# Kernel tuning notes

Measured on AMD Instinct MI355X. Metric: run time of the kernel, lower is better.

## Reference

```python
import jax, jax.numpy as jnp
import numpy as np

SOBEL_X = jnp.array([[-1., 0., 1.], [-2., 0., 2.], [-1., 0., 1.]], dtype=jnp.float32).reshape(1, 1, 3, 3)
SOBEL_Y = jnp.array([[-1., -2., -1.], [0., 0., 0.], [1., 2., 1.]], dtype=jnp.float32).reshape(1, 1, 3, 3)
KERNEL_MASK = jnp.ones((1, 1, 3, 3), dtype=jnp.float32)


def _conv(x, k):
    # x: (N,1,H,W), k: (1,1,3,3), SAME padding (matches torch padding=1)
    return jax.lax.conv_general_dilated(
        x, k, window_strides=(1, 1), padding='SAME',
        dimension_numbers=('NCHW', 'OIHW', 'NCHW'))


def setup_inputs() -> dict:
    key = jax.random.key(0)
    k1, k2, k3 = jax.random.split(key, 3)
    shape = (2, 6, 512, 512, 8)  # (B, T, H, W, F)
    prediction = jax.random.normal(k1, shape, dtype=jnp.float32)
    target = jax.random.normal(k2, shape, dtype=jnp.float32)
    mask = jax.random.randint(k3, shape, 0, 2, dtype=jnp.int32)
    return {"prediction": prediction, "target": target, "mask": mask}


def reference(prediction, target, mask):
    B, T, H, W, F = prediction.shape
    # (B,T,H,W,F) -> (B*T*F, 1, H, W)
    def to_nchw(x):
        return x.transpose(0, 1, 4, 2, 3).reshape(B * T * F, 1, H, W)

    mask_r = to_nchw(mask.astype(jnp.float32))
    pred_r = to_nchw(prediction)
    tgt_r = to_nchw(target)

    valid = (_conv(mask_r, KERNEL_MASK) == 9.0).astype(prediction.dtype)

    gx_p = _conv(pred_r, SOBEL_X) * valid
    gy_p = _conv(pred_r, SOBEL_Y) * valid
    gx_t = _conv(tgt_r, SOBEL_X) * valid
    gy_t = _conv(tgt_r, SOBEL_Y) * valid

    # mode == 'l1'
    loss = jnp.abs(gx_p - gx_t) + jnp.abs(gy_p - gy_t)
    # (B*T*F,1,H,W) -> (B,T,H,W,F)
    return loss.reshape(B, T, F, H, W).transpose(0, 1, 3, 4, 2)
```

## Files before the change

kernel.cpp:

```cpp
#include <hip/hip_runtime.h>


constexpr int H = 512, W = 512, F = 8;
constexpr int IMAGES = 12;
constexpr int SPAN  = 128;
constexpr int NSPAN = W / SPAN;
constexpr int ORWS  = 6;
constexpr int SRWS  = 8;
constexpr int STRIPS = (H + ORWS - 1) / ORWS;
constexpr int NB = IMAGES * NSPAN * STRIPS;
constexpr int UROW = 2 * SPAN + 4;

typedef float f32x4 __attribute__((ext_vector_type(4)));

__global__ __launch_bounds__(512) void sobel_loss_kernel(
    const float* __restrict__ pred,
    const float* __restrict__ tgt,
    const int*   __restrict__ mask,
    float*       __restrict__ out)
{
    __shared__ float4         dls[SRWS * UROW];
    __shared__ unsigned short mls[SRWS * UROW];

    const int tid  = threadIdx.x;
    const int l    = tid & 63;
    const int wv   = tid >> 6;

    const int b0  = blockIdx.x;
    const int bid = (b0 & 7) * (NB >> 3) + (b0 >> 3);

    const int img   = bid / (NSPAN * STRIPS);
    const int rest  = bid - img * (NSPAN * STRIPS);
    const int span  = rest / STRIPS;
    const int strip = rest - span * STRIPS;

    const int r0 = strip * ORWS;
    const int w0 = span * SPAN;

    const size_t ibase = (size_t)img * ((size_t)H * W * F);

    {
        const int gr  = r0 - 1 + wv;
        const int grc = gr < 0 ? 0 : (gr >= H ? H - 1 : gr);
        const bool rv = (gr >= 0) & (gr < H);
        const size_t rowf = ibase + (size_t)grc * (W * F) + (size_t)w0 * F;

        float4 P[4], T[4]; int4 M[4];
#pragma unroll
        for (int k = 0; k < 4; ++k) {
            const size_t o = rowf + (size_t)k * 256 + l * 4;
            P[k] = *(const float4*)(pred + o);
            T[k] = *(const float4*)(tgt  + o);
            M[k] = *(const int4*)(mask + o);
        }

        float4 EP = make_float4(0.f,0.f,0.f,0.f), ET = EP;
        int4   EM = make_int4(0,0,0,0);
        const bool left = (l < 2);
        const int  qe   = l & 1;
        const int  pxg  = left ? (w0 - 1) : (w0 + SPAN);
        const bool ib   = (pxg >= 0) & (pxg < W);
        if (l < 4) {
            const int pxc = ib ? pxg : 0;
            const size_t o = ibase + (size_t)grc * (W * F) + (size_t)pxc * F + qe * 4;
            EP = *(const float4*)(pred + o);
            ET = *(const float4*)(tgt  + o);
            EM = *(const int4*)(mask + o);
        }

        float4* drow = dls + wv * UROW;
        unsigned short* mrow = mls + wv * UROW;
#pragma unroll
        for (int k = 0; k < 4; ++k) {
            const int u = 2 + k * 64 + l;
            drow[u] = make_float4(P[k].x - T[k].x, P[k].y - T[k].y,
                                  P[k].z - T[k].z, P[k].w - T[k].w);
            const unsigned bits = (unsigned)(M[k].x | (M[k].y << 1) |
                                             (M[k].z << 2) | (M[k].w << 3));
            mrow[u] = (unsigned short)(rv ? bits : 0u);
        }
        if (l < 4) {
            const int u = left ? qe : (2 + 2 * SPAN + qe);
            drow[u] = make_float4(EP.x - ET.x, EP.y - ET.y,
                                  EP.z - ET.z, EP.w - ET.w);
            const unsigned bits = (unsigned)(EM.x | (EM.y << 1) |
                                             (EM.z << 2) | (EM.w << 3));
            mrow[u] = (unsigned short)((rv && ib) ? bits : 0u);
        }
    }

    __syncthreads();

#pragma unroll
    for (int pass = 0; pass < 3; ++pass) {
        const int ot = tid + pass * 512;
        const int ol = ot >> 8;
        const int uo = ot & 255;
        const int ro = r0 + ol;
        if (ro < H) {
            const int bc = (ol + 1) * UROW + 2 + uo;

            const float4 a0 = dls[bc - UROW - 2];
            const float4 a1 = dls[bc - UROW];
            const float4 a2 = dls[bc - UROW + 2];
            const unsigned mA = (unsigned)mls[bc - UROW - 2] &
                                (unsigned)mls[bc - UROW] &
                                (unsigned)mls[bc - UROW + 2];
            const float4 b0r = dls[bc - 2];
            const float4 b1r = dls[bc];
            const float4 b2r = dls[bc + 2];
            const unsigned mB = (unsigned)mls[bc - 2] &
                                (unsigned)mls[bc] &
                                (unsigned)mls[bc + 2];
            const float4 c0 = dls[bc + UROW - 2];
            const float4 c1 = dls[bc + UROW];
            const float4 c2 = dls[bc + UROW + 2];
            const unsigned mC = (unsigned)mls[bc + UROW - 2] &
                                (unsigned)mls[bc + UROW] &
                                (unsigned)mls[bc + UROW + 2];

            const unsigned vm = mA & mB & mC;

            f32x4 o;
#define COMP(cc, bit)                                                          \
            {                                                                  \
                const float hx0 = a2.cc - a0.cc;                               \
                const float hx1 = b2r.cc - b0r.cc;                             \
                const float hx2 = c2.cc - c0.cc;                               \
                const float hs0 = a0.cc + 2.f * a1.cc + a2.cc;                 \
                const float hs2 = c0.cc + 2.f * c1.cc + c2.cc;                 \
                const float gx = hx0 + 2.f * hx1 + hx2;                        \
                const float gy = hs2 - hs0;                                    \
                o.cc = (vm & (1u << bit)) ? (fabsf(gx) + fabsf(gy)) : 0.f;     \
            }
            COMP(x, 0) COMP(y, 1) COMP(z, 2) COMP(w, 3)
#undef COMP

            float* const op = out + ibase + ((size_t)ro * W + w0) * F + uo * 4;
            __builtin_nontemporal_store(o, (f32x4*)op);
        }
    }
}

extern "C" void kernel_launch(void* const* d_in, const int* in_sizes, int n_in,
                              void* d_out, int out_size, void* d_ws, size_t ws_size,
                              hipStream_t stream) {
    const float* pred = (const float*)d_in[0];
    const float* tgt  = (const float*)d_in[1];
    const int*   mask = (const int*)d_in[2];
    float*       out  = (float*)d_out;

    sobel_loss_kernel<<<NB, 512, 0, stream>>>(pred, tgt, mask, out);
}
```

Before: 314.2 us.

## Stream rows through shared-memory ring buffer with register prefetch per block

Replaces the one-shot strip kernel, which reloads two halo rows for every six output rows, with blocks that walk 64-row vertical chunks of a 64-pixel span. Input rows go into a 10-slot shared ring, and the next rows are prefetched into registers while the current rows are computed. This cuts redundant halo reads from about 33% to about 3% and overlaps global loads with compute. In exchange it adds two barriers per iteration, launches fewer and smaller blocks (768 blocks of 256 threads), and uses ordinary stores in place of nontemporal ones.

```diff
diff --git a/kernel.cpp b/kernel.cpp
--- a/kernel.cpp
+++ b/kernel.cpp
@@ -3,129 +3,154 @@
 
 constexpr int H = 512, W = 512, F = 8;
 constexpr int IMAGES = 12;
-constexpr int SPAN  = 128;
+constexpr int SPAN  = 64;
 constexpr int NSPAN = W / SPAN;
-constexpr int ORWS  = 6;
-constexpr int SRWS  = 8;
-constexpr int STRIPS = (H + ORWS - 1) / ORWS;
-constexpr int NB = IMAGES * NSPAN * STRIPS;
-constexpr int UROW = 2 * SPAN + 4;
+constexpr int VCH   = 64;
+constexpr int NVCH  = H / VCH;
+constexpr int NB    = IMAGES * NSPAN * NVCH;
+constexpr int RING  = 10;
+constexpr int STEP  = 8;
+constexpr int ITERS = VCH / STEP;
+constexpr int UROW  = 2 * SPAN + 4;
 
 typedef float f32x4 __attribute__((ext_vector_type(4)));
 
-__global__ __launch_bounds__(512) void sobel_loss_kernel(
+struct RowReg {
+    float4 p0, p1, t0, t1, hp, ht;
+    int4   m0, m1, hm;
+};
+
+__device__ __forceinline__ int pack4(const int4 m) {
+    return m.x | (m.y << 1) | (m.z << 2) | (m.w << 3);
+}
+
+__device__ __forceinline__ float4 sub4(const float4 a, const float4 b) {
+    return make_float4(a.x - b.x, a.y - b.y, a.z - b.z, a.w - b.w);
+}
+
+__device__ __forceinline__ void row_load(
+    RowReg& R, const float* __restrict__ pred, const float* __restrict__ tgt,
+    const int* __restrict__ mask, size_t ibase, int gr, int w0, int l)
+{
+    const int grc = gr < 0 ? 0 : (gr > H - 1 ? H - 1 : gr);
+    const size_t rb = ibase + (size_t)grc * (W * F) + (size_t)w0 * F;
+    const int lo = l * 4;
+    R.p0 = *(const float4*)(pred + rb + lo);
+    R.p1 = *(const float4*)(pred + rb + lo + 256);
+    R.t0 = *(const float4*)(tgt  + rb + lo);
+    R.t1 = *(const float4*)(tgt  + rb + lo + 256);
+    R.m0 = *(const int4*)(mask + rb + lo);
+    R.m1 = *(const int4*)(mask + rb + lo + 256);
+    R.hp = make_float4(0.f, 0.f, 0.f, 0.f);
+    R.ht = R.hp;
+    R.hm = make_int4(0, 0, 0, 0);
+    if (l < 4) {
+        const int side = l >> 1, hq = l & 1;
+        const int px  = side ? w0 + SPAN : w0 - 1;
+        const int pxc = px < 0 ? 0 : (px > W - 1 ? W - 1 : px);
+        const size_t hb = ibase + (size_t)grc * (W * F) + (size_t)pxc * F + hq * 4;
+        R.hp = *(const float4*)(pred + hb);
+        R.ht = *(const float4*)(tgt  + hb);
+        R.hm = *(const int4*)(mask + hb);
+    }
+}
+
+__device__ __forceinline__ void row_write(
+    const RowReg& R, float4* __restrict__ dls, unsigned* __restrict__ mls,
+    int slot, int gr, int w0, int l)
+{
+    const bool rv = (gr >= 0) & (gr < H);
+    float4*   drow = dls + slot * UROW;
+    unsigned* mrow = mls + slot * UROW;
+    drow[2 + l]  = sub4(R.p0, R.t0);
+    drow[66 + l] = sub4(R.p1, R.t1);
+    mrow[2 + l]  = rv ? (unsigned)pack4(R.m0) : 0u;
+    mrow[66 + l] = rv ? (unsigned)pack4(R.m1) : 0u;
+    if (l < 4) {
+        const int side = l >> 1, hq = l & 1;
+        const int px = side ? w0 + SPAN : w0 - 1;
+        const bool ib = (px >= 0) & (px < W);
+        const int u = side ? (2 + 2 * SPAN + hq) : hq;
+        drow[u] = sub4(R.hp, R.ht);
+        mrow[u] = (rv && ib) ? (unsigned)pack4(R.hm) : 0u;
+    }
+}
+
+__global__ __launch_bounds__(256, 3) void sobel_loss_kernel(
     const float* __restrict__ pred,
     const float* __restrict__ tgt,
     const int*   __restrict__ mask,
     float*       __restrict__ out)
 {
-    __shared__ float4         dls[SRWS * UROW];
-    __shared__ unsigned short mls[SRWS * UROW];
+    __shared__ float4   dls[RING * UROW];
+    __shared__ unsigned mls[RING * UROW];
 
-    const int tid  = threadIdx.x;
-    const int l    = tid & 63;
-    const int wv   = tid >> 6;
+    const int tid = threadIdx.x;
+    const int l   = tid & 63;
+    const int wv  = tid >> 6;
 
-    const int b0  = blockIdx.x;
-    const int bid = (b0 & 7) * (NB >> 3) + (b0 >> 3);
-
-    const int img   = bid / (NSPAN * STRIPS);
-    const int rest  = bid - img * (NSPAN * STRIPS);
-    const int span  = rest / STRIPS;
-    const int strip = rest - span * STRIPS;
-
-    const int r0 = strip * ORWS;
-    const int w0 = span * SPAN;
+    const int bid  = blockIdx.x;
+    const int img  = bid >> 6;
+    const int rest = bid & 63;
+    const int span = rest >> 3;
+    const int vch  = rest & 7;
+    const int w0   = span * SPAN;
+    const int v0   = vch * VCH;
 
     const size_t ibase = (size_t)img * ((size_t)H * W * F);
 
-    {
-        const int gr  = r0 - 1 + wv;
-        const int grc = gr < 0 ? 0 : (gr >= H ? H - 1 : gr);
-        const bool rv = (gr >= 0) & (gr < H);
-        const size_t rowf = ibase + (size_t)grc * (W * F) + (size_t)w0 * F;
-
-        float4 P[4], T[4]; int4 M[4];
-#pragma unroll
-        for (int k = 0; k < 4; ++k) {
-            const size_t o = rowf + (size_t)k * 256 + l * 4;
-            P[k] = *(const float4*)(pred + o);
-            T[k] = *(const float4*)(tgt  + o);
-            M[k] = *(const int4*)(mask + o);
-        }
-
-        float4 EP = make_float4(0.f,0.f,0.f,0.f), ET = EP;
-        int4   EM = make_int4(0,0,0,0);
-        const bool left = (l < 2);
-        const int  qe   = l & 1;
-        const int  pxg  = left ? (w0 - 1) : (w0 + SPAN);
-        const bool ib   = (pxg >= 0) & (pxg < W);
-        if (l < 4) {
-            const int pxc = ib ? pxg : 0;
-            const size_t o = ibase + (size_t)grc * (W * F) + (size_t)pxc * F + qe * 4;
-            EP = *(const float4*)(pred + o);
-            ET = *(const float4*)(tgt  + o);
-            EM = *(const int4*)(mask + o);
-        }
-
-        float4* drow = dls + wv * UROW;
-        unsigned short* mrow = mls + wv * UROW;
-#pragma unroll
-        for (int k = 0; k < 4; ++k) {
-            const int u = 2 + k * 64 + l;
-            drow[u] = make_float4(P[k].x - T[k].x, P[k].y - T[k].y,
-                                  P[k].z - T[k].z, P[k].w - T[k].w);
-            const unsigned bits = (unsigned)(M[k].x | (M[k].y << 1) |
-                                             (M[k].z << 2) | (M[k].w << 3));
-            mrow[u] = (unsigned short)(rv ? bits : 0u);
-        }
-        if (l < 4) {
-            const int u = left ? qe : (2 + 2 * SPAN + qe);
-            drow[u] = make_float4(EP.x - ET.x, EP.y - ET.y,
-                                  EP.z - ET.z, EP.w - ET.w);
-            const unsigned bits = (unsigned)(EM.x | (EM.y << 1) |
-                                             (EM.z << 2) | (EM.w << 3));
-            mrow[u] = (unsigned short)((rv && ib) ? bits : 0u);
-        }
+    for (int j = wv; j < RING; j += 4) {
+        RowReg R;
+        row_load(R, pred, tgt, mask, ibase, v0 - 1 + j, w0, l);
+        row_write(R, dls, mls, j, v0 - 1 + j, w0, l);
     }
-
     __syncthreads();
 
+    int bs = 0;
+    for (int k = 0; k < ITERS; ++k) {
+        const bool more = (k + 1) < ITERS;
+        const int  ja = 2 * wv, jb = 2 * wv + 1;
+        const int  gra = v0 + STEP * k + 9 + ja;
+        const int  grb = v0 + STEP * k + 9 + jb;
+
+        RowReg RA, RB;
+        if (more) {
+            row_load(RA, pred, tgt, mask, ibase, gra, w0, l);
+            row_load(RB, pred, tgt, mask, ibase, grb, w0, l);
+        }
+        __builtin_amdgcn_sched_barrier(0);
+
+        const int o0 = v0 + STEP * k;
 #pragma unroll
-    for (int pass = 0; pass < 3; ++pass) {
-        const int ot = tid + pass * 512;
-        const int ol = ot >> 8;
-        const int uo = ot & 255;
-        const int ro = r0 + ol;
-        if (ro < H) {
-            const int bc = (ol + 1) * UROW + 2 + uo;
+        for (int p = 0; p < 4; ++p) {
+            const int item = tid + 256 * p;
+            const int lr = item >> 7;
+            const int uo = item & 127;
+            int sB = bs + lr + 1; if (sB >= RING) sB -= RING;
+            int sA = sB - 1;      if (sA < 0)     sA += RING;
+            int sC = sB + 1;      if (sC >= RING) sC -= RING;
+            const int cu = 2 + uo;
 
-            const float4 a0 = dls[bc - UROW - 2];
-            const float4 a1 = dls[bc - UROW];
-            const float4 a2 = dls[bc - UROW + 2];
-            const unsigned mA = (unsigned)mls[bc - UROW - 2] &
-                                (unsigned)mls[bc - UROW] &
-                                (unsigned)mls[bc - UROW + 2];
-            const float4 b0r = dls[bc - 2];
-            const float4 b1r = dls[bc];
-            const float4 b2r = dls[bc + 2];
-            const unsigned mB = (unsigned)mls[bc - 2] &
-                                (unsigned)mls[bc] &
-                                (unsigned)mls[bc + 2];
-            const float4 c0 = dls[bc + UROW - 2];
-            const float4 c1 = dls[bc + UROW];
-            const float4 c2 = dls[bc + UROW + 2];
-            const unsigned mC = (unsigned)mls[bc + UROW - 2] &
-                                (unsigned)mls[bc + UROW] &
-                                (unsigned)mls[bc + UROW + 2];
+            const float4 a0 = dls[sA * UROW + cu - 2];
+            const float4 a1 = dls[sA * UROW + cu];
+            const float4 a2 = dls[sA * UROW + cu + 2];
+            const float4 b0 = dls[sB * UROW + cu - 2];
+            const float4 b1 = dls[sB * UROW + cu];
+            const float4 b2 = dls[sB * UROW + cu + 2];
+            const float4 c0 = dls[sC * UROW + cu - 2];
+            const float4 c1 = dls[sC * UROW + cu];
+            const float4 c2 = dls[sC * UROW + cu + 2];
 
-            const unsigned vm = mA & mB & mC;
+            const unsigned vm =
+                mls[sA * UROW + cu - 2] & mls[sA * UROW + cu] & mls[sA * UROW + cu + 2] &
+                mls[sB * UROW + cu - 2] & mls[sB * UROW + cu] & mls[sB * UROW + cu + 2] &
+                mls[sC * UROW + cu - 2] & mls[sC * UROW + cu] & mls[sC * UROW + cu + 2];
 
             f32x4 o;
 #define COMP(cc, bit)                                                          \
             {                                                                  \
                 const float hx0 = a2.cc - a0.cc;                               \
-                const float hx1 = b2r.cc - b0r.cc;                             \
+                const float hx1 = b2.cc - b0.cc;                               \
                 const float hx2 = c2.cc - c0.cc;                               \
                 const float hs0 = a0.cc + 2.f * a1.cc + a2.cc;                 \
                 const float hs2 = c0.cc + 2.f * c1.cc + c2.cc;                 \
@@ -136,9 +161,20 @@
             COMP(x, 0) COMP(y, 1) COMP(z, 2) COMP(w, 3)
 #undef COMP
 
-            float* const op = out + ibase + ((size_t)ro * W + w0) * F + uo * 4;
-            __builtin_nontemporal_store(o, (f32x4*)op);
+            *(f32x4*)(out + ibase + (size_t)(o0 + lr) * (W * F)
+                          + (size_t)w0 * F + uo * 4) = o;
         }
+
+        __syncthreads();
+        if (more) {
+            int wsA = bs + ja; if (wsA >= RING) wsA -= RING;
+            int wsB = bs + jb; if (wsB >= RING) wsB -= RING;
+            row_write(RA, dls, mls, wsA, gra, w0, l);
+            row_write(RB, dls, mls, wsB, grb, w0, l);
+        }
+        __syncthreads();
+
+        bs += STEP; if (bs >= RING) bs -= RING;
     }
 }
 
@@ -150,5 +186,5 @@
     const int*   mask = (const int*)d_in[2];
     float*       out  = (float*)d_out;
 
-    sobel_loss_kernel<<<NB, 512, 0, stream>>>(pred, tgt, mask, out);
+    sobel_loss_kernel<<<NB, 256, 0, stream>>>(pred, tgt, mask, out);
 }
```

After: 310.5 us. About the same (-1.2%).
